# Kernel tuning notes

Measured on AMD Instinct MI355X. Metric: run time of the kernel, lower is better.

## Reference

```python
import jax, jax.numpy as jnp
import numpy as np

HIDDEN = 2048
T = 8192
WASHOUT = 200
SPECTRAL_RADIUS = 0.9


def setup_inputs() -> dict:
    key = jax.random.key(0)
    k_u, k_in, k_res, k_out = jax.random.split(key, 4)
    u = jax.random.normal(k_u, (T,), dtype=jnp.float32)
    # w_in ~ Uniform(-0.5, 0.5) * input_scaling (1.0)
    w_in = jax.random.uniform(k_in, (HIDDEN,), dtype=jnp.float32) - 0.5
    # w_res ~ Uniform(-0.5, 0.5), rescaled to spectral radius 0.9 (init-time buffer construction)
    w_res = np.asarray(jax.random.uniform(k_res, (HIDDEN, HIDDEN), dtype=jnp.float32)) - 0.5
    sr = float(np.max(np.abs(np.linalg.eigvals(w_res.astype(np.float64)))))
    w_res = jnp.asarray((w_res * (SPECTRAL_RADIUS / sr)).astype(np.float32))
    # trained readout stand-in (module stores it as buffer w_out, used by pinv predict path)
    w_out = jax.random.normal(k_out, (HIDDEN,), dtype=jnp.float32) * 0.05
    return {"u": u, "w_in": w_in, "w_res": w_res, "w_out": w_out}


def reference(u, w_in, w_res, w_out):
    # x_{t} = tanh(w_in * u_t + w_res @ x_{t-1}), x_{-1} = 0
    def step(x, u_t):
        x = jnp.tanh(w_in * u_t + w_res @ x)
        return x, x

    x0 = jnp.zeros((HIDDEN,), dtype=w_res.dtype)
    _, X = jax.lax.scan(step, x0, u)  # X: [T, HIDDEN]
    # pinv predict path: X[washout:] @ w_out
    return X[WASHOUT:] @ w_out
```

## Files before the change

kernel.cpp:

```cpp
#include <hip/hip_runtime.h>

#define HIDDEN   2048
#define T_STEPS  8192
#define WASHOUT  200
#define NWG      64
#define NTHR     1024
#define NWAVE    (NTHR / 64)
#define ROWS_PER_WG   (HIDDEN / NWG)
#define ROWS_PER_WAVE (ROWS_PER_WG / NWAVE)
#define NCHUNK   16
#define NREPL    8
#define REPL     (2 * HIDDEN)


#define DPP_ADD(x, ctrl) ((x) + __int_as_float(__builtin_amdgcn_update_dpp( \
    0, __float_as_int(x), ctrl, 0xF, 0xF, true)))

typedef unsigned uint4v __attribute__((ext_vector_type(4)));
typedef unsigned uint2v __attribute__((ext_vector_type(2)));

#define PERMLANE_SUM_1632(h)                                         \
  {                                                                  \
    uint2v s16 = __builtin_amdgcn_permlane16_swap(                   \
        __float_as_uint(h), __float_as_uint(h), false, false);       \
    h = __uint_as_float(s16.x) + __uint_as_float(s16.y);             \
    uint2v s32 = __builtin_amdgcn_permlane32_swap(                   \
        __float_as_uint(h), __float_as_uint(h), false, false);       \
    h = __uint_as_float(s32.x) + __uint_as_float(s32.y);             \
  }

__global__ __launch_bounds__(NTHR, 1) void esn_main(
    const float* __restrict__ u,
    const float* __restrict__ w_in,
    const float* __restrict__ w_res,
    const float* __restrict__ w_out,
    float* __restrict__ out,
    unsigned long long* __restrict__ pairs,
    int nrepl)
{
  const int g  = blockIdx.x;
  const int j  = threadIdx.x;
  const int wv = j >> 6;
  const int l  = j & 63;

  unsigned xcc;
  asm("s_getreg_b32 %0, hwreg(HW_REG_XCC_ID)" : "=s"(xcc));
  const unsigned ri = xcc & (unsigned)(nrepl - 1);
  unsigned long long* __restrict__ myrep = pairs + (size_t)ri * REPL;

  __shared__ float x_s[2][HIDDEN];
  __shared__ float u_s[T_STEPS];
  __shared__ float fresh[ROWS_PER_WG];

#pragma unroll
  for (int k = 0; k < T_STEPS / NTHR; ++k) u_s[j + NTHR * k] = u[j + NTHR * k];

  const int r0 = g * ROWS_PER_WG + wv * ROWS_PER_WAVE;

  float wreg[ROWS_PER_WAVE][2 * NCHUNK];
#pragma unroll
  for (int i = 0; i < ROWS_PER_WAVE; ++i) {
#pragma unroll
    for (int c = 0; c < NCHUNK; ++c) {
      const float2 a = *(const float2*)&w_res[(r0 + i) * HIDDEN + c * 128 + 2 * l];
      wreg[i][2 * c + 0] = a.x; wreg[i][2 * c + 1] = a.y;
    }
  }

  const float winl = w_in[r0 + (l & 1)];
  const float wol  = (wv == 8 && l < 32) ? w_out[g * 32 + l] : 0.f;

  __syncthreads();

  for (int t = 0; t < T_STEPS; ++t) {
#pragma unroll
    for (int i = 0; i < ROWS_PER_WAVE; ++i)
#pragma unroll
      for (int k = 0; k < 2 * NCHUNK; ++k)
        asm volatile("" : "+v"(wreg[i][k]));

    float d0 = 0.f, d1 = 0.f;
    const unsigned b = (unsigned)((t - 1) & 1);
    if (t > 0) {
      const unsigned want = (unsigned)(t - 1);
      const unsigned long long* bp = myrep + b * HIDDEN + (wv << 7) + 2 * l;
      uint4v A;
      for (;;) {
        asm volatile(
            "global_load_dwordx4 %0, %1, off sc1\n\t"
            "s_waitcnt vmcnt(0)"
            : "=&v"(A)
            : "v"(bp)
            : "memory");
        if ((A.x == want) & (A.z == want)) break;
      }
      float2 xv;
      xv.x = __uint_as_float(A.y);
      xv.y = __uint_as_float(A.w);
      *(float2*)&x_s[b][(wv << 7) + 2 * l] = xv;
    }
    __syncthreads();

    if (t > 0) {
#pragma unroll
      for (int c = 0; c < NCHUNK; ++c) {
        const float2 x2 = *(const float2*)&x_s[b][(c << 7) + 2 * l];
        d0 = fmaf(wreg[0][2 * c + 0], x2.x, d0);
        d0 = fmaf(wreg[0][2 * c + 1], x2.y, d0);
        d1 = fmaf(wreg[1][2 * c + 0], x2.x, d1);
        d1 = fmaf(wreg[1][2 * c + 1], x2.y, d1);
      }
    }

    float e0 = DPP_ADD(d0, 0xB1);
    float e1 = DPP_ADD(d1, 0xB1);
    float h = (l & 1) ? e1 : e0;
    h = DPP_ADD(h, 0x4E);
    h = DPP_ADD(h, 0x124);
    h = DPP_ADD(h, 0x128);
    PERMLANE_SUM_1632(h)

    const float ut = u_s[t];
    if (l < ROWS_PER_WAVE) {
      const float a = fmaf(winl, ut, h);
      float z;
      asm("v_exp_f32 %0, %1" : "=v"(z) : "v"(a * 2.885390082f));
      float r;
      asm("v_rcp_f32 %0, %1" : "=v"(r) : "v"(z + 1.0f));
      fresh[wv * ROWS_PER_WAVE + l] = fmaf(-2.0f, r, 1.0f);
    }
    __syncthreads();

    if (wv < nrepl && l < ROWS_PER_WG) {
      const unsigned long long pk =
          ((unsigned long long)__float_as_uint(fresh[l]) << 32) | (unsigned)t;
      __hip_atomic_store(
          pairs + (size_t)wv * REPL + (t & 1) * HIDDEN + g * ROWS_PER_WG + l,
          pk, __ATOMIC_RELAXED, __HIP_MEMORY_SCOPE_AGENT);
    }
    if (wv == 8 && t >= WASHOUT) {
      float part = (l < 32) ? fresh[l] * wol : 0.f;
      part = DPP_ADD(part, 0xB1);
      part = DPP_ADD(part, 0x4E);
      part = DPP_ADD(part, 0x124);
      part = DPP_ADD(part, 0x128);
      PERMLANE_SUM_1632(part)
      if (l == 0) atomicAdd(&out[t - WASHOUT], part);
    }
  }
}

extern "C" void kernel_launch(void* const* d_in, const int* in_sizes, int n_in,
                              void* d_out, int out_size, void* d_ws, size_t ws_size,
                              hipStream_t stream) {
  const float* u     = (const float*)d_in[0];
  const float* w_in  = (const float*)d_in[1];
  const float* w_res = (const float*)d_in[2];
  const float* w_out = (const float*)d_in[3];
  float* out = (float*)d_out;
  unsigned long long* pairs = (unsigned long long*)d_ws;

  const int nrepl =
      (ws_size >= (size_t)NREPL * REPL * sizeof(unsigned long long)) ? NREPL : 1;

  hipMemsetAsync(out, 0, (size_t)out_size * sizeof(float), stream);
  esn_main<<<NWG, NTHR, 0, stream>>>(u, w_in, w_res, w_out, out, pairs, nrepl);
}
```

Baseline: 14.60 ms.

## Split recurrence across 128 smaller workgroups with float4 state exchange

Doubles the number of workgroups and halves threads per workgroup. Each wave still owns two rows but now covers 256 columns per chunk using float4 weight registers, two dwordx4 polling loads, and float4 LDS reads. This is meant to shorten the per-step critical path: each barrier spans fewer waves and each CU does less FMA work. The register-pinning asm barrier is also moved out of the time loop. The trade-off is more workgroups spin-polling the shared exchange buffer, and the compiler is now free to spill or reload weights inside the loop.

```diff
diff --git a/kernel.cpp b/kernel.cpp
--- a/kernel.cpp
+++ b/kernel.cpp
@@ -3,12 +3,12 @@
 #define HIDDEN   2048
 #define T_STEPS  8192
 #define WASHOUT  200
-#define NWG      64
-#define NTHR     1024
+#define NWG      128
+#define NTHR     512
 #define NWAVE    (NTHR / 64)
 #define ROWS_PER_WG   (HIDDEN / NWG)
 #define ROWS_PER_WAVE (ROWS_PER_WG / NWAVE)
-#define NCHUNK   16
+#define NCHUNK   8
 #define NREPL    8
 #define REPL     (2 * HIDDEN)
 
@@ -57,58 +57,68 @@
 
   const int r0 = g * ROWS_PER_WG + wv * ROWS_PER_WAVE;
 
-  float wreg[ROWS_PER_WAVE][2 * NCHUNK];
+  float wreg[ROWS_PER_WAVE][4 * NCHUNK];
 #pragma unroll
   for (int i = 0; i < ROWS_PER_WAVE; ++i) {
 #pragma unroll
     for (int c = 0; c < NCHUNK; ++c) {
-      const float2 a = *(const float2*)&w_res[(r0 + i) * HIDDEN + c * 128 + 2 * l];
-      wreg[i][2 * c + 0] = a.x; wreg[i][2 * c + 1] = a.y;
+      const float4 a = *(const float4*)&w_res[(r0 + i) * HIDDEN + c * 256 + 4 * l];
+      wreg[i][4 * c + 0] = a.x; wreg[i][4 * c + 1] = a.y;
+      wreg[i][4 * c + 2] = a.z; wreg[i][4 * c + 3] = a.w;
     }
   }
+#pragma unroll
+  for (int i = 0; i < ROWS_PER_WAVE; ++i)
+#pragma unroll
+    for (int k = 0; k < 4 * NCHUNK; ++k)
+      asm volatile("" : "+v"(wreg[i][k]));
 
   const float winl = w_in[r0 + (l & 1)];
-  const float wol  = (wv == 8 && l < 32) ? w_out[g * 32 + l] : 0.f;
+  const float wol  = (wv == 1 && l < ROWS_PER_WG)
+                     ? w_out[g * ROWS_PER_WG + l] : 0.f;
 
   __syncthreads();
 
   for (int t = 0; t < T_STEPS; ++t) {
-#pragma unroll
-    for (int i = 0; i < ROWS_PER_WAVE; ++i)
-#pragma unroll
-      for (int k = 0; k < 2 * NCHUNK; ++k)
-        asm volatile("" : "+v"(wreg[i][k]));
-
     float d0 = 0.f, d1 = 0.f;
     const unsigned b = (unsigned)((t - 1) & 1);
     if (t > 0) {
       const unsigned want = (unsigned)(t - 1);
-      const unsigned long long* bp = myrep + b * HIDDEN + (wv << 7) + 2 * l;
-      uint4v A;
+      const unsigned long long* bp = myrep + b * HIDDEN + (wv << 8) + 4 * l;
+      uint4v A, B;
       for (;;) {
         asm volatile(
-            "global_load_dwordx4 %0, %1, off sc1\n\t"
+            "global_load_dwordx4 %0, %2, off sc1\n\t"
+            "global_load_dwordx4 %1, %3, off sc1\n\t"
             "s_waitcnt vmcnt(0)"
-            : "=&v"(A)
-            : "v"(bp)
+            : "=&v"(A), "=&v"(B)
+            : "v"(bp), "v"(bp + 2)
             : "memory");
-        if ((A.x == want) & (A.z == want)) break;
+        if (((A.x == want) & (A.z == want)) &
+            ((B.x == want) & (B.z == want))) break;
       }
-      float2 xv;
+      float4 xv;
       xv.x = __uint_as_float(A.y);
       xv.y = __uint_as_float(A.w);
-      *(float2*)&x_s[b][(wv << 7) + 2 * l] = xv;
+      xv.z = __uint_as_float(B.y);
+      xv.w = __uint_as_float(B.w);
+      *(float4*)&x_s[b][(wv << 8) + 4 * l] = xv;
     }
     __syncthreads();
 
     if (t > 0) {
+      const float4* xs4 = (const float4*)x_s[b];
 #pragma unroll
       for (int c = 0; c < NCHUNK; ++c) {
-        const float2 x2 = *(const float2*)&x_s[b][(c << 7) + 2 * l];
-        d0 = fmaf(wreg[0][2 * c + 0], x2.x, d0);
-        d0 = fmaf(wreg[0][2 * c + 1], x2.y, d0);
-        d1 = fmaf(wreg[1][2 * c + 0], x2.x, d1);
-        d1 = fmaf(wreg[1][2 * c + 1], x2.y, d1);
+        const float4 x4 = xs4[(c << 6) + l];
+        d0 = fmaf(wreg[0][4 * c + 0], x4.x, d0);
+        d0 = fmaf(wreg[0][4 * c + 1], x4.y, d0);
+        d0 = fmaf(wreg[0][4 * c + 2], x4.z, d0);
+        d0 = fmaf(wreg[0][4 * c + 3], x4.w, d0);
+        d1 = fmaf(wreg[1][4 * c + 0], x4.x, d1);
+        d1 = fmaf(wreg[1][4 * c + 1], x4.y, d1);
+        d1 = fmaf(wreg[1][4 * c + 2], x4.z, d1);
+        d1 = fmaf(wreg[1][4 * c + 3], x4.w, d1);
       }
     }
 
@@ -138,8 +148,8 @@
           pairs + (size_t)wv * REPL + (t & 1) * HIDDEN + g * ROWS_PER_WG + l,
           pk, __ATOMIC_RELAXED, __HIP_MEMORY_SCOPE_AGENT);
     }
-    if (wv == 8 && t >= WASHOUT) {
-      float part = (l < 32) ? fresh[l] * wol : 0.f;
+    if (wv == 1 && t >= WASHOUT) {
+      float part = (l < ROWS_PER_WG) ? fresh[l] * wol : 0.f;
       part = DPP_ADD(part, 0xB1);
       part = DPP_ADD(part, 0x4E);
       part = DPP_ADD(part, 0x124);
```

Result: slower. 16.62 ms (+13.8%).
